# Kernel optimization log

Measured on AMD Instinct MI355X. Metric: run time of the kernel, lower is better.

The kernel has to match this reference:

```python
import jax, jax.numpy as jnp
import numpy as np

N, E, IN, C, H = 50000, 1600000, 128, 64, 2
HC = H * C  # 128; num_out = 128, conv_out channels per head = 64
NEG_SLOPE = 0.2


def setup_inputs() -> dict:
    key = jax.random.key(0)
    ks = jax.random.split(key, 16)
    x = jax.random.normal(ks[0], (N, IN), dtype=jnp.float32)
    edge_index = jax.random.randint(ks[1], (2, E), 0, N, dtype=jnp.int64)

    def gat_params(k, fan_in, heads, out_ch):
        k1, k2, k3 = jax.random.split(k, 3)
        sc = 1.0 / np.sqrt(fan_in)
        W = jax.random.normal(k1, (fan_in, heads * out_ch), dtype=jnp.float32) * sc
        a_src = jax.random.normal(k2, (heads, out_ch), dtype=jnp.float32) * 0.1
        a_dst = jax.random.normal(k3, (heads, out_ch), dtype=jnp.float32) * 0.1
        b = jnp.zeros((heads * out_ch,), dtype=jnp.float32)
        return W, a_src, a_dst, b

    W_in, a_src_in, a_dst_in, b_in = gat_params(ks[2], IN, H, C)
    # 2 hidden layers, stacked on leading axis
    Wh, ash, adh, bh = [], [], [], []
    for i in range(2):
        W, a_s, a_d, b = gat_params(ks[3 + i], HC, H, C)
        Wh.append(W); ash.append(a_s); adh.append(a_d); bh.append(b)
    W_h = jnp.stack(Wh); a_src_h = jnp.stack(ash)
    a_dst_h = jnp.stack(adh); b_h = jnp.stack(bh)
    W_out, a_src_out, a_dst_out, b_out = gat_params(ks[6], HC, H, C)
    return dict(x=x, edge_index=edge_index,
                W_in=W_in, a_src_in=a_src_in, a_dst_in=a_dst_in, b_in=b_in,
                W_h=W_h, a_src_h=a_src_h, a_dst_h=a_dst_h, b_h=b_h,
                W_out=W_out, a_src_out=a_src_out, a_dst_out=a_dst_out, b_out=b_out)


def gat_layer(xf, src, dst, W, a_src, a_dst, b, heads, out_ch):
    n = xf.shape[0]
    h = (xf @ W).reshape(n, heads, out_ch)              # [N,H,C]
    e_src = jnp.einsum('nhc,hc->nh', h, a_src)          # [N,H]
    e_dst = jnp.einsum('nhc,hc->nh', h, a_dst)
    e = jax.nn.leaky_relu(e_src[src] + e_dst[dst], NEG_SLOPE)  # [E',H]
    m = jax.ops.segment_max(e, dst, num_segments=n)     # softmax over edges per dst
    p = jnp.exp(e - m[dst])
    s = jax.ops.segment_sum(p, dst, num_segments=n)
    alpha = p / (s[dst] + 1e-16)
    out = jax.ops.segment_sum(alpha[:, :, None] * h[src], dst, num_segments=n)
    return out.reshape(n, heads * out_ch) + b


def reference(x, edge_index, W_in, a_src_in, a_dst_in, b_in,
              W_h, a_src_h, a_dst_h, b_h,
              W_out, a_src_out, a_dst_out, b_out):
    # add self loops (PyG GATConv default add_self_loops=True)
    loops = jnp.arange(N, dtype=edge_index.dtype)
    src = jnp.concatenate([edge_index[0], loops])
    dst = jnp.concatenate([edge_index[1], loops])

    h = jax.nn.relu(gat_layer(x, src, dst, W_in, a_src_in, a_dst_in, b_in, H, C))
    for i in range(2):
        h = jax.nn.relu(gat_layer(h, src, dst, W_h[i], a_src_h[i], a_dst_h[i], b_h[i], H, C))
    out = gat_layer(h, src, dst, W_out, a_src_out, a_dst_out, b_out, H, C)
    return out
```

## Files before the change

### kernel.cpp

```cpp
#include <hip/hip_runtime.h>

#define NNODES 50000
#define NEDGES 1600000
#define NEG_SLOPE 0.2f

#define SCAN_NB 256
#define SCAN_CH 196

typedef __attribute__((ext_vector_type(8))) short short8;
typedef __attribute__((ext_vector_type(4))) float f32x4;
typedef __attribute__((ext_vector_type(4))) unsigned short us4;

static __device__ __forceinline__ unsigned short f2bf(float f) {
    unsigned u = __float_as_uint(f);
    unsigned r = u + 0x7FFFu + ((u >> 16) & 1u);
    return (unsigned short)(r >> 16);
}
static __device__ __forceinline__ float bf2f(unsigned short h) {
    return __uint_as_float(((unsigned)h) << 16);
}
static __device__ __forceinline__ unsigned short f2h(float f) {
    union { _Float16 x; unsigned short u; } c;
    c.x = (_Float16)f;
    return c.u;
}
static __device__ __forceinline__ float h2f(unsigned short u) {
    union { unsigned short u; _Float16 x; } c;
    c.u = u;
    return (float)c.x;
}


__global__ void k_count(const int* __restrict__ ei, int* __restrict__ count,
                        int* __restrict__ pos) {
    int t = blockIdx.x * blockDim.x + threadIdx.x;
    int stride = gridDim.x * blockDim.x;
    #pragma unroll
    for (int i = 0; i < 8; i++) {
        int e = t + i * stride;
        if (e < NEDGES) pos[e] = atomicAdd(&count[ei[NEDGES + e]], 1);
    }
}

__global__ __launch_bounds__(256) void k_bsum(const int* __restrict__ count,
                                              int* __restrict__ bsum) {
    __shared__ int red[4];
    int t = threadIdx.x, b = blockIdx.x;
    int idx = b * SCAN_CH + t;
    int v = (t < SCAN_CH && idx < NNODES) ? count[idx] + 1 : 0;
    #pragma unroll
    for (int m = 1; m <= 32; m <<= 1) v += __shfl_xor(v, m);
    if ((t & 63) == 0) red[t >> 6] = v;
    __syncthreads();
    if (t == 0) bsum[b] = red[0] + red[1] + red[2] + red[3];
}

__global__ __launch_bounds__(256) void k_bscan(const int* __restrict__ bsum,
                                               int* __restrict__ boff,
                                               int* __restrict__ row_ptr) {
    __shared__ int s[256];
    int t = threadIdx.x;
    int v = bsum[t];
    s[t] = v;
    __syncthreads();
    for (int off = 1; off < 256; off <<= 1) {
        int u = (t >= off) ? s[t - off] : 0;
        __syncthreads();
        s[t] += u;
        __syncthreads();
    }
    boff[t] = s[t] - v;
    if (t == 255) row_ptr[NNODES] = s[255];
}

__global__ __launch_bounds__(256) void k_rowptr(const int* __restrict__ count,
                                                const int* __restrict__ boff,
                                                int* __restrict__ row_ptr,
                                                int* __restrict__ csr_src) {
    __shared__ int s[256];
    int t = threadIdx.x, b = blockIdx.x;
    int idx = b * SCAN_CH + t;
    bool valid = (t < SCAN_CH && idx < NNODES);
    int v = valid ? count[idx] + 1 : 0;
    s[t] = v;
    __syncthreads();
    for (int off = 1; off < 256; off <<= 1) {
        int u = (t >= off) ? s[t - off] : 0;
        __syncthreads();
        s[t] += u;
        __syncthreads();
    }
    if (valid) {
        int run = boff[b] + s[t] - v;
        row_ptr[idx] = run;
        csr_src[run] = idx;
    }
}

__global__ void k_scatter(const int* __restrict__ ei, const int* __restrict__ row_ptr,
                          const int* __restrict__ pos, int* __restrict__ csr_src) {
    int t = blockIdx.x * blockDim.x + threadIdx.x;
    int stride = gridDim.x * blockDim.x;
    #pragma unroll
    for (int i = 0; i < 4; i++) {
        int e = t + i * stride;
        if (e < NEDGES) {
            int s = ei[e];
            int d = ei[NEDGES + e];
            __builtin_nontemporal_store(s, &csr_src[row_ptr[d] + 1 + pos[e]]);
        }
    }
}


__global__ void k_split(const float* __restrict__ x, unsigned short* __restrict__ hi,
                        unsigned short* __restrict__ lo) {
    int i = blockIdx.x * blockDim.x + threadIdx.x;
    if (i >= NNODES * 128 / 4) return;
    float4 v = *(const float4*)(x + (size_t)i * 4);
    unsigned short h0 = f2bf(v.x), h1 = f2bf(v.y), h2 = f2bf(v.z), h3 = f2bf(v.w);
    *(ushort4*)(hi + (size_t)i * 4) = make_ushort4(h0, h1, h2, h3);
    *(ushort4*)(lo + (size_t)i * 4) =
        make_ushort4(f2bf(v.x - bf2f(h0)), f2bf(v.y - bf2f(h1)),
                     f2bf(v.z - bf2f(h2)), f2bf(v.w - bf2f(h3)));
}

__global__ __launch_bounds__(256, 2) void k_gemm_mfma(
        const unsigned short* __restrict__ Ahi, const unsigned short* __restrict__ Alo,
        const float* __restrict__ W,
        const float* __restrict__ a_src, const float* __restrict__ a_dst,
        unsigned short* __restrict__ Hh,
        float* __restrict__ e_src, float* __restrict__ e_dst)
{
    __shared__ __align__(16) short sAhi[128 * 128];
    __shared__ __align__(16) short sAlo[128 * 128];
    __shared__ float eS[4][128];
    __shared__ float eD[4][128];

    const int tid  = threadIdx.x;
    const int lane = tid & 63;
    const int w    = tid >> 6;
    const int l15  = lane & 15;
    const int quad = lane >> 4;
    const int row0 = blockIdx.x * 128;

    short8 Bh[2][4], Bl[2][4];
    for (int nt = 0; nt < 2; nt++) {
        int n = w * 32 + nt * 16 + l15;
        for (int ks = 0; ks < 4; ks++) {
            short8 bh, bl;
            #pragma unroll
            for (int j = 0; j < 8; j++) {
                float wv = W[(size_t)(ks * 32 + quad * 8 + j) * 128 + n];
                unsigned short h = f2bf(wv);
                bh[j] = (short)h;
                bl[j] = (short)f2bf(wv - bf2f(h));
            }
            Bh[nt][ks] = bh; Bl[nt][ks] = bl;
        }
    }

    for (int i = tid; i < 2048; i += 256) {
        int m  = i >> 4;
        int kc = i & 15;
        int g  = row0 + m; if (g > NNODES - 1) g = NNODES - 1;
        int cp = kc ^ (m & 15);
        short8 vh = *(const short8*)(Ahi + (size_t)g * 128 + kc * 8);
        short8 vl = *(const short8*)(Alo + (size_t)g * 128 + kc * 8);
        *(short8*)&sAhi[m * 128 + cp * 8] = vh;
        *(short8*)&sAlo[m * 128 + cp * 8] = vl;
    }
    __syncthreads();

    f32x4 zero = {0.f, 0.f, 0.f, 0.f};
    f32x4 acc[8][2];
    #pragma unroll
    for (int mt = 0; mt < 8; mt++) { acc[mt][0] = zero; acc[mt][1] = zero; }

    #pragma unroll
    for (int mt = 0; mt < 8; mt++) {
        int m = mt * 16 + l15;
        #pragma unroll
        for (int ks = 0; ks < 4; ks++) {
            int kc = ks * 4 + quad;
            int cp = kc ^ l15;
            short8 ah = *(const short8*)&sAhi[m * 128 + cp * 8];
            short8 al = *(const short8*)&sAlo[m * 128 + cp * 8];
            #pragma unroll
            for (int nt = 0; nt < 2; nt++) {
                acc[mt][nt] = __builtin_amdgcn_mfma_f32_16x16x32_bf16(ah, Bh[nt][ks], acc[mt][nt], 0, 0, 0);
                acc[mt][nt] = __builtin_amdgcn_mfma_f32_16x16x32_bf16(al, Bh[nt][ks], acc[mt][nt], 0, 0, 0);
                acc[mt][nt] = __builtin_amdgcn_mfma_f32_16x16x32_bf16(ah, Bl[nt][ks], acc[mt][nt], 0, 0, 0);
            }
        }
    }

    float as0 = a_src[w * 32 + l15],      ad0 = a_dst[w * 32 + l15];
    float as1 = a_src[w * 32 + 16 + l15], ad1 = a_dst[w * 32 + 16 + l15];
    #pragma unroll
    for (int mt = 0; mt < 8; mt++) {
        #pragma unroll
        for (int r = 0; r < 4; r++) {
            int m = mt * 16 + quad * 4 + r;
            int g = row0 + m;
            float v0 = acc[mt][0][r], v1 = acc[mt][1][r];
            if (g < NNODES) {
                int n0 = w * 32 + l15;
                Hh[(size_t)g * 128 + n0]      = f2h(v0);
                Hh[(size_t)g * 128 + n0 + 16] = f2h(v1);
            }
            float ps = v0 * as0 + v1 * as1;
            float pd = v0 * ad0 + v1 * ad1;
            ps += __shfl_xor(ps, 1); ps += __shfl_xor(ps, 2);
            ps += __shfl_xor(ps, 4); ps += __shfl_xor(ps, 8);
            pd += __shfl_xor(pd, 1); pd += __shfl_xor(pd, 2);
            pd += __shfl_xor(pd, 4); pd += __shfl_xor(pd, 8);
            if (l15 == 0) { eS[w][m] = ps; eD[w][m] = pd; }
        }
    }
    __syncthreads();
    {
        int m = tid >> 1, head = tid & 1;
        int g = row0 + m;
        if (g < NNODES) {
            e_src[g * 2 + head] = eS[head * 2][m] + eS[head * 2 + 1][m];
            e_dst[g * 2 + head] = eD[head * 2][m] + eD[head * 2 + 1][m];
        }
    }
}

__global__ __launch_bounds__(256) void k_aggregate_h(const unsigned short* __restrict__ Hh,
                                                     const float* __restrict__ e_src,
                                                     const float* __restrict__ e_dst,
                                                     const int* __restrict__ row_ptr,
                                                     const int* __restrict__ csr_src,
                                                     const float* __restrict__ bias,
                                                     unsigned short* __restrict__ ohi,
                                                     unsigned short* __restrict__ olo) {
    int lane = threadIdx.x & 63;
    int wv   = threadIdx.x >> 6;
    int d    = blockIdx.x * 4 + wv;
    if (d >= NNODES) return;
    int half = lane >> 5;
    int li   = lane & 31;
    int head = li >> 4;
    int c0   = li * 4;
    float ed = e_dst[d * 2 + head];
    int beg = row_ptr[d], end = row_ptr[d + 1];
    f32x4 acc = {0.f, 0.f, 0.f, 0.f};
    float ssum = 0.f;
    int j = beg;
    for (; j + 16 <= end; j += 16) {
        int s[8];
        #pragma unroll
        for (int u = 0; u < 8; u++) s[u] = csr_src[j + 2 * u + half];
        us4 q[8];
        #pragma unroll
        for (int u = 0; u < 8; u++) q[u] = *(const us4*)(Hh + (size_t)s[u] * 128 + c0);
        float p[8];
        #pragma unroll
        for (int u = 0; u < 8; u++) {
            float t = e_src[s[u] * 2 + head] + ed;
            t = t > 0.f ? t : NEG_SLOPE * t;
            p[u] = __expf(t);
        }
        #pragma unroll
        for (int u = 0; u < 8; u++) {
            acc[0] += p[u] * h2f(q[u][0]);
            acc[1] += p[u] * h2f(q[u][1]);
            acc[2] += p[u] * h2f(q[u][2]);
            acc[3] += p[u] * h2f(q[u][3]);
            ssum   += p[u];
        }
    }
    for (; j < end; j += 2) {
        int idx = j + half;
        bool valid = idx < end;
        int s = csr_src[valid ? idx : end - 1];
        float t = e_src[s * 2 + head] + ed;
        t = t > 0.f ? t : NEG_SLOPE * t;
        float p = valid ? __expf(t) : 0.f;
        us4 q = *(const us4*)(Hh + (size_t)s * 128 + c0);
        acc[0] += p * h2f(q[0]);
        acc[1] += p * h2f(q[1]);
        acc[2] += p * h2f(q[2]);
        acc[3] += p * h2f(q[3]);
        ssum   += p;
    }
    acc[0] += __shfl_xor(acc[0], 32);
    acc[1] += __shfl_xor(acc[1], 32);
    acc[2] += __shfl_xor(acc[2], 32);
    acc[3] += __shfl_xor(acc[3], 32);
    ssum   += __shfl_xor(ssum,   32);
    if (half == 0) {
        float inv = 1.0f / ssum;
        float4 bv = *(const float4*)(bias + c0);
        float o0 = fmaxf(acc[0] * inv + bv.x, 0.f);
        float o1 = fmaxf(acc[1] * inv + bv.y, 0.f);
        float o2 = fmaxf(acc[2] * inv + bv.z, 0.f);
        float o3 = fmaxf(acc[3] * inv + bv.w, 0.f);
        unsigned short h0 = f2bf(o0), h1 = f2bf(o1), h2 = f2bf(o2), h3 = f2bf(o3);
        *(ushort4*)&ohi[(size_t)d * 128 + c0] = make_ushort4(h0, h1, h2, h3);
        *(ushort4*)&olo[(size_t)d * 128 + c0] =
            make_ushort4(f2bf(o0 - bf2f(h0)), f2bf(o1 - bf2f(h1)),
                         f2bf(o2 - bf2f(h2)), f2bf(o3 - bf2f(h3)));
    }
}

__global__ __launch_bounds__(256) void k_aggregate_f(const unsigned short* __restrict__ Hh,
                                                     const float* __restrict__ e_src,
                                                     const float* __restrict__ e_dst,
                                                     const int* __restrict__ row_ptr,
                                                     const int* __restrict__ csr_src,
                                                     const float* __restrict__ bias,
                                                     float* __restrict__ outf) {
    int lane = threadIdx.x & 63;
    int wv   = threadIdx.x >> 6;
    int d    = blockIdx.x * 4 + wv;
    if (d >= NNODES) return;
    int half = lane >> 5;
    int li   = lane & 31;
    int head = li >> 4;
    int c0   = li * 4;
    float ed = e_dst[d * 2 + head];
    int beg = row_ptr[d], end = row_ptr[d + 1];
    f32x4 acc = {0.f, 0.f, 0.f, 0.f};
    float ssum = 0.f;
    int j = beg;
    for (; j + 16 <= end; j += 16) {
        int s[8];
        #pragma unroll
        for (int u = 0; u < 8; u++) s[u] = csr_src[j + 2 * u + half];
        us4 q[8];
        #pragma unroll
        for (int u = 0; u < 8; u++) q[u] = *(const us4*)(Hh + (size_t)s[u] * 128 + c0);
        float p[8];
        #pragma unroll
        for (int u = 0; u < 8; u++) {
            float t = e_src[s[u] * 2 + head] + ed;
            t = t > 0.f ? t : NEG_SLOPE * t;
            p[u] = __expf(t);
        }
        #pragma unroll
        for (int u = 0; u < 8; u++) {
            acc[0] += p[u] * h2f(q[u][0]);
            acc[1] += p[u] * h2f(q[u][1]);
            acc[2] += p[u] * h2f(q[u][2]);
            acc[3] += p[u] * h2f(q[u][3]);
            ssum   += p[u];
        }
    }
    for (; j < end; j += 2) {
        int idx = j + half;
        bool valid = idx < end;
        int s = csr_src[valid ? idx : end - 1];
        float t = e_src[s * 2 + head] + ed;
        t = t > 0.f ? t : NEG_SLOPE * t;
        float p = valid ? __expf(t) : 0.f;
        us4 q = *(const us4*)(Hh + (size_t)s * 128 + c0);
        acc[0] += p * h2f(q[0]);
        acc[1] += p * h2f(q[1]);
        acc[2] += p * h2f(q[2]);
        acc[3] += p * h2f(q[3]);
        ssum   += p;
    }
    acc[0] += __shfl_xor(acc[0], 32);
    acc[1] += __shfl_xor(acc[1], 32);
    acc[2] += __shfl_xor(acc[2], 32);
    acc[3] += __shfl_xor(acc[3], 32);
    ssum   += __shfl_xor(ssum,   32);
    if (half == 0) {
        float inv = 1.0f / ssum;
        float4 bv = *(const float4*)(bias + c0);
        *(float4*)(outf + (size_t)d * 128 + c0) =
            make_float4(acc[0] * inv + bv.x, acc[1] * inv + bv.y,
                        acc[2] * inv + bv.z, acc[3] * inv + bv.w);
    }
}


extern "C" void kernel_launch(void* const* d_in, const int* in_sizes, int n_in,
                              void* d_out, int out_size, void* d_ws, size_t ws_size,
                              hipStream_t stream) {
    const float* x  = (const float*)d_in[0];
    const int*   ei = (const int*)d_in[1];

    char* ws = (char*)d_ws;
    size_t off = 0;
    auto alloc = [&](size_t bytes) {
        void* p = ws + off;
        off = (off + bytes + 255) & ~(size_t)255;
        return p;
    };
    int*            count   = (int*)alloc((size_t)NNODES * 4);
    int*            row_ptr = (int*)alloc((size_t)(NNODES + 1) * 4);
    int*            csr     = (int*)alloc((size_t)(NEDGES + NNODES) * 4);
    int*            pos     = (int*)alloc((size_t)NEDGES * 4);
    int*            bsum    = (int*)alloc((size_t)SCAN_NB * 4);
    int*            boff    = (int*)alloc((size_t)SCAN_NB * 4);
    unsigned short* hh      = (unsigned short*)alloc((size_t)NNODES * 128 * 2);
    float*          es      = (float*)alloc((size_t)NNODES * 2 * 4);
    float*          edv     = (float*)alloc((size_t)NNODES * 2 * 4);
    (void)ws_size; (void)in_sizes; (void)n_in; (void)out_size;

    unsigned short* hi = (unsigned short*)d_out;
    unsigned short* lo = hi + (size_t)NNODES * 128;

    hipMemsetAsync(count, 0, (size_t)NNODES * 4, stream);
    k_count  <<<(NEDGES + 8 * 256 - 1) / (8 * 256), 256, 0, stream>>>(ei, count, pos);
    k_bsum   <<<SCAN_NB, 256, 0, stream>>>(count, bsum);
    k_bscan  <<<1, 256, 0, stream>>>(bsum, boff, row_ptr);
    k_rowptr <<<SCAN_NB, 256, 0, stream>>>(count, boff, row_ptr, csr);
    k_scatter<<<(NEDGES + 4 * 256 - 1) / (4 * 256), 256, 0, stream>>>(ei, row_ptr, pos, csr);
    k_split  <<<(NNODES * 128 / 4 + 255) / 256, 256, 0, stream>>>(x, hi, lo);

    const float* W_h = (const float*)d_in[6];
    const float* ash = (const float*)d_in[7];
    const float* adh = (const float*)d_in[8];
    const float* bh  = (const float*)d_in[9];

    struct Layer { const float *W, *as, *ad, *b; };
    Layer L[4] = {
        { (const float*)d_in[2],  (const float*)d_in[3],  (const float*)d_in[4],  (const float*)d_in[5]  },
        { W_h,              ash,        adh,        bh        },
        { W_h + 128 * 128,  ash + 128,  adh + 128,  bh + 128  },
        { (const float*)d_in[10], (const float*)d_in[11], (const float*)d_in[12], (const float*)d_in[13] },
    };

    const int gemm_blocks = (NNODES + 127) / 128;
    const int agg_blocks  = (NNODES + 3) / 4;
    for (int l = 0; l < 4; l++) {
        k_gemm_mfma<<<gemm_blocks, 256, 0, stream>>>(hi, lo, L[l].W, L[l].as, L[l].ad,
                                                     hh, es, edv);
        if (l < 3) {
            k_aggregate_h<<<agg_blocks, 256, 0, stream>>>(hh, es, edv, row_ptr, csr,
                                                          L[l].b, hi, lo);
        } else {
            k_aggregate_f<<<agg_blocks, 256, 0, stream>>>(hh, es, edv, row_ptr, csr,
                                                          L[l].b, (float*)d_out);
        }
    }
}
```

Measured before the change: 596.4 us.

## Precompute bf16 split weights once, fuse input split into GEMM, persistent 64-row tiles

Adds a one-time kernel that converts all four layers' weights into transposed bf16 hi/lo pairs. Each GEMM block can then load its B fragments with vector loads instead of doing strided fp32 loads and conversions per block. The standalone x split kernel is removed and the first layer converts x to hi/lo inside the GEMM tile load. The GEMM now uses 64-row tiles in a grid-stride loop over 768 blocks with higher occupancy. This saves a full pass over x and the repeated weight conversion, at the cost of extra syncs per tile and a launch that loops.

```diff
diff --git a/kernel.cpp b/kernel.cpp
--- a/kernel.cpp
+++ b/kernel.cpp
@@ -6,6 +6,10 @@
 
 #define SCAN_NB 256
 #define SCAN_CH 196
+
+#define MT_ROWS 64
+#define NMT 782
+#define GEMM_BLOCKS 768
 
 typedef __attribute__((ext_vector_type(8))) short short8;
 typedef __attribute__((ext_vector_type(4))) float f32x4;
@@ -112,120 +116,135 @@
     }
 }
 
-
-__global__ void k_split(const float* __restrict__ x, unsigned short* __restrict__ hi,
-                        unsigned short* __restrict__ lo) {
-    int i = blockIdx.x * blockDim.x + threadIdx.x;
-    if (i >= NNODES * 128 / 4) return;
-    float4 v = *(const float4*)(x + (size_t)i * 4);
-    unsigned short h0 = f2bf(v.x), h1 = f2bf(v.y), h2 = f2bf(v.z), h3 = f2bf(v.w);
-    *(ushort4*)(hi + (size_t)i * 4) = make_ushort4(h0, h1, h2, h3);
-    *(ushort4*)(lo + (size_t)i * 4) =
-        make_ushort4(f2bf(v.x - bf2f(h0)), f2bf(v.y - bf2f(h1)),
-                     f2bf(v.z - bf2f(h2)), f2bf(v.w - bf2f(h3)));
-}
-
-__global__ __launch_bounds__(256, 2) void k_gemm_mfma(
+__global__ __launch_bounds__(256) void k_wprep(const float* __restrict__ W0,
+                                               const float* __restrict__ Wh,
+                                               const float* __restrict__ Wout,
+                                               unsigned short* __restrict__ wthi,
+                                               unsigned short* __restrict__ wtlo) {
+    int t = blockIdx.x * blockDim.x + threadIdx.x;
+    int l = t >> 14;
+    int i = t & 16383;
+    int k = i >> 7, n = i & 127;
+    const float* src = (l == 0) ? W0 : (l == 3) ? Wout : (Wh + (size_t)(l - 1) * 16384);
+    float v = src[i];
+    unsigned short h = f2bf(v);
+    wthi[(size_t)l * 16384 + n * 128 + k] = h;
+    wtlo[(size_t)l * 16384 + n * 128 + k] = f2bf(v - bf2f(h));
+}
+
+__global__ __launch_bounds__(256, 3) void k_gemm_mfma(
+        const float* __restrict__ X,
         const unsigned short* __restrict__ Ahi, const unsigned short* __restrict__ Alo,
-        const float* __restrict__ W,
+        const unsigned short* __restrict__ Wthi, const unsigned short* __restrict__ Wtlo,
         const float* __restrict__ a_src, const float* __restrict__ a_dst,
         unsigned short* __restrict__ Hh,
-        float* __restrict__ e_src, float* __restrict__ e_dst)
+        float* __restrict__ e_src, float* __restrict__ e_dst, int use_x)
 {
-    __shared__ __align__(16) short sAhi[128 * 128];
-    __shared__ __align__(16) short sAlo[128 * 128];
-    __shared__ float eS[4][128];
-    __shared__ float eD[4][128];
+    __shared__ __align__(16) short sAhi[MT_ROWS * 128];
+    __shared__ __align__(16) short sAlo[MT_ROWS * 128];
+    __shared__ float eS[4][MT_ROWS];
+    __shared__ float eD[4][MT_ROWS];
 
     const int tid  = threadIdx.x;
     const int lane = tid & 63;
     const int w    = tid >> 6;
     const int l15  = lane & 15;
     const int quad = lane >> 4;
-    const int row0 = blockIdx.x * 128;
 
     short8 Bh[2][4], Bl[2][4];
+    #pragma unroll
     for (int nt = 0; nt < 2; nt++) {
         int n = w * 32 + nt * 16 + l15;
+        #pragma unroll
         for (int ks = 0; ks < 4; ks++) {
-            short8 bh, bl;
-            #pragma unroll
-            for (int j = 0; j < 8; j++) {
-                float wv = W[(size_t)(ks * 32 + quad * 8 + j) * 128 + n];
-                unsigned short h = f2bf(wv);
-                bh[j] = (short)h;
-                bl[j] = (short)f2bf(wv - bf2f(h));
-            }
-            Bh[nt][ks] = bh; Bl[nt][ks] = bl;
-        }
-    }
-
-    for (int i = tid; i < 2048; i += 256) {
-        int m  = i >> 4;
-        int kc = i & 15;
-        int g  = row0 + m; if (g > NNODES - 1) g = NNODES - 1;
-        int cp = kc ^ (m & 15);
-        short8 vh = *(const short8*)(Ahi + (size_t)g * 128 + kc * 8);
-        short8 vl = *(const short8*)(Alo + (size_t)g * 128 + kc * 8);
-        *(short8*)&sAhi[m * 128 + cp * 8] = vh;
-        *(short8*)&sAlo[m * 128 + cp * 8] = vl;
-    }
-    __syncthreads();
-
-    f32x4 zero = {0.f, 0.f, 0.f, 0.f};
-    f32x4 acc[8][2];
-    #pragma unroll
-    for (int mt = 0; mt < 8; mt++) { acc[mt][0] = zero; acc[mt][1] = zero; }
-
-    #pragma unroll
-    for (int mt = 0; mt < 8; mt++) {
-        int m = mt * 16 + l15;
-        #pragma unroll
-        for (int ks = 0; ks < 4; ks++) {
-            int kc = ks * 4 + quad;
-            int cp = kc ^ l15;
-            short8 ah = *(const short8*)&sAhi[m * 128 + cp * 8];
-            short8 al = *(const short8*)&sAlo[m * 128 + cp * 8];
-            #pragma unroll
-            for (int nt = 0; nt < 2; nt++) {
-                acc[mt][nt] = __builtin_amdgcn_mfma_f32_16x16x32_bf16(ah, Bh[nt][ks], acc[mt][nt], 0, 0, 0);
-                acc[mt][nt] = __builtin_amdgcn_mfma_f32_16x16x32_bf16(al, Bh[nt][ks], acc[mt][nt], 0, 0, 0);
-                acc[mt][nt] = __builtin_amdgcn_mfma_f32_16x16x32_bf16(ah, Bl[nt][ks], acc[mt][nt], 0, 0, 0);
-            }
-        }
-    }
-
+            Bh[nt][ks] = *(const short8*)(Wthi + (size_t)n * 128 + ks * 32 + quad * 8);
+            Bl[nt][ks] = *(const short8*)(Wtlo + (size_t)n * 128 + ks * 32 + quad * 8);
+        }
+    }
     float as0 = a_src[w * 32 + l15],      ad0 = a_dst[w * 32 + l15];
     float as1 = a_src[w * 32 + 16 + l15], ad1 = a_dst[w * 32 + 16 + l15];
-    #pragma unroll
-    for (int mt = 0; mt < 8; mt++) {
-        #pragma unroll
-        for (int r = 0; r < 4; r++) {
-            int m = mt * 16 + quad * 4 + r;
+
+    for (int mt0 = blockIdx.x; mt0 < NMT; mt0 += GEMM_BLOCKS) {
+        const int row0 = mt0 * MT_ROWS;
+
+        for (int i = tid; i < MT_ROWS * 16; i += 256) {
+            int m  = i >> 4;
+            int kc = i & 15;
+            int g  = row0 + m; if (g > NNODES - 1) g = NNODES - 1;
+            int cp = kc ^ (m & 15);
+            short8 vh, vl;
+            if (use_x) {
+                float4 xa = *(const float4*)(X + (size_t)g * 128 + kc * 8);
+                float4 xb = *(const float4*)(X + (size_t)g * 128 + kc * 8 + 4);
+                float xs[8] = {xa.x, xa.y, xa.z, xa.w, xb.x, xb.y, xb.z, xb.w};
+                #pragma unroll
+                for (int q = 0; q < 8; q++) {
+                    unsigned short h = f2bf(xs[q]);
+                    vh[q] = (short)h;
+                    vl[q] = (short)f2bf(xs[q] - bf2f(h));
+                }
+            } else {
+                vh = *(const short8*)(Ahi + (size_t)g * 128 + kc * 8);
+                vl = *(const short8*)(Alo + (size_t)g * 128 + kc * 8);
+            }
+            *(short8*)&sAhi[m * 128 + cp * 8] = vh;
+            *(short8*)&sAlo[m * 128 + cp * 8] = vl;
+        }
+        __syncthreads();
+
+        f32x4 zero = {0.f, 0.f, 0.f, 0.f};
+        f32x4 acc[4][2];
+        #pragma unroll
+        for (int mt = 0; mt < 4; mt++) { acc[mt][0] = zero; acc[mt][1] = zero; }
+        #pragma unroll
+        for (int mt = 0; mt < 4; mt++) {
+            int m = mt * 16 + l15;
+            #pragma unroll
+            for (int ks = 0; ks < 4; ks++) {
+                int kc = ks * 4 + quad;
+                int cp = kc ^ l15;
+                short8 ah = *(const short8*)&sAhi[m * 128 + cp * 8];
+                short8 al = *(const short8*)&sAlo[m * 128 + cp * 8];
+                #pragma unroll
+                for (int nt = 0; nt < 2; nt++) {
+                    acc[mt][nt] = __builtin_amdgcn_mfma_f32_16x16x32_bf16(ah, Bh[nt][ks], acc[mt][nt], 0, 0, 0);
+                    acc[mt][nt] = __builtin_amdgcn_mfma_f32_16x16x32_bf16(al, Bh[nt][ks], acc[mt][nt], 0, 0, 0);
+                    acc[mt][nt] = __builtin_amdgcn_mfma_f32_16x16x32_bf16(ah, Bl[nt][ks], acc[mt][nt], 0, 0, 0);
+                }
+            }
+        }
+
+        #pragma unroll
+        for (int mt = 0; mt < 4; mt++) {
+            #pragma unroll
+            for (int r = 0; r < 4; r++) {
+                int m = mt * 16 + quad * 4 + r;
+                int g = row0 + m;
+                float v0 = acc[mt][0][r], v1 = acc[mt][1][r];
+                if (g < NNODES) {
+                    int n0 = w * 32 + l15;
+                    Hh[(size_t)g * 128 + n0]      = f2h(v0);
+                    Hh[(size_t)g * 128 + n0 + 16] = f2h(v1);
+                }
+                float ps = v0 * as0 + v1 * as1;
+                float pd = v0 * ad0 + v1 * ad1;
+                ps += __shfl_xor(ps, 1); ps += __shfl_xor(ps, 2);
+                ps += __shfl_xor(ps, 4); ps += __shfl_xor(ps, 8);
+                pd += __shfl_xor(pd, 1); pd += __shfl_xor(pd, 2);
+                pd += __shfl_xor(pd, 4); pd += __shfl_xor(pd, 8);
+                if (l15 == 0) { eS[w][m] = ps; eD[w][m] = pd; }
+            }
+        }
+        __syncthreads();
+        if (tid < MT_ROWS * 2) {
+            int m = tid >> 1, head = tid & 1;
             int g = row0 + m;
-            float v0 = acc[mt][0][r], v1 = acc[mt][1][r];
             if (g < NNODES) {
-                int n0 = w * 32 + l15;
-                Hh[(size_t)g * 128 + n0]      = f2h(v0);
-                Hh[(size_t)g * 128 + n0 + 16] = f2h(v1);
+                e_src[g * 2 + head] = eS[head * 2][m] + eS[head * 2 + 1][m];
+                e_dst[g * 2 + head] = eD[head * 2][m] + eD[head * 2 + 1][m];
             }
-            float ps = v0 * as0 + v1 * as1;
-            float pd = v0 * ad0 + v1 * ad1;
-            ps += __shfl_xor(ps, 1); ps += __shfl_xor(ps, 2);
-            ps += __shfl_xor(ps, 4); ps += __shfl_xor(ps, 8);
-            pd += __shfl_xor(pd, 1); pd += __shfl_xor(pd, 2);
-            pd += __shfl_xor(pd, 4); pd += __shfl_xor(pd, 8);
-            if (l15 == 0) { eS[w][m] = ps; eD[w][m] = pd; }
-        }
-    }
-    __syncthreads();
-    {
-        int m = tid >> 1, head = tid & 1;
-        int g = row0 + m;
-        if (g < NNODES) {
-            e_src[g * 2 + head] = eS[head * 2][m] + eS[head * 2 + 1][m];
-            e_dst[g * 2 + head] = eD[head * 2][m] + eD[head * 2 + 1][m];
-        }
+        }
+        __syncthreads();
     }
 }
 
@@ -399,6 +418,8 @@
     int*            bsum    = (int*)alloc((size_t)SCAN_NB * 4);
     int*            boff    = (int*)alloc((size_t)SCAN_NB * 4);
     unsigned short* hh      = (unsigned short*)alloc((size_t)NNODES * 128 * 2);
+    unsigned short* wthi    = (unsigned short*)alloc((size_t)4 * 16384 * 2);
+    unsigned short* wtlo    = (unsigned short*)alloc((size_t)4 * 16384 * 2);
     float*          es      = (float*)alloc((size_t)NNODES * 2 * 4);
     float*          edv     = (float*)alloc((size_t)NNODES * 2 * 4);
     (void)ws_size; (void)in_sizes; (void)n_in; (void)out_size;
@@ -406,32 +427,35 @@
     unsigned short* hi = (unsigned short*)d_out;
     unsigned short* lo = hi + (size_t)NNODES * 128;
 
+    const float* W0   = (const float*)d_in[2];
+    const float* W_h  = (const float*)d_in[6];
+    const float* Wout = (const float*)d_in[10];
+
     hipMemsetAsync(count, 0, (size_t)NNODES * 4, stream);
     k_count  <<<(NEDGES + 8 * 256 - 1) / (8 * 256), 256, 0, stream>>>(ei, count, pos);
+    k_wprep  <<<256, 256, 0, stream>>>(W0, W_h, Wout, wthi, wtlo);
     k_bsum   <<<SCAN_NB, 256, 0, stream>>>(count, bsum);
     k_bscan  <<<1, 256, 0, stream>>>(bsum, boff, row_ptr);
     k_rowptr <<<SCAN_NB, 256, 0, stream>>>(count, boff, row_ptr, csr);
     k_scatter<<<(NEDGES + 4 * 256 - 1) / (4 * 256), 256, 0, stream>>>(ei, row_ptr, pos, csr);
-    k_split  <<<(NNODES * 128 / 4 + 255) / 256, 256, 0, stream>>>(x, hi, lo);
-
-    const float* W_h = (const float*)d_in[6];
+
     const float* ash = (const float*)d_in[7];
     const float* adh = (const float*)d_in[8];
     const float* bh  = (const float*)d_in[9];
 
-    struct Layer { const float *W, *as, *ad, *b; };
+    struct Layer { const float *as, *ad, *b; };
     Layer L[4] = {
-        { (const float*)d_in[2],  (const float*)d_in[3],  (const float*)d_in[4],  (const float*)d_in[5]  },
-        { W_h,              ash,        adh,        bh        },
-        { W_h + 128 * 128,  ash + 128,  adh + 128,  bh + 128  },
-        { (const float*)d_in[10], (const float*)d_in[11], (const float*)d_in[12], (const float*)d_in[13] },
+        { (const float*)d_in[3],  (const float*)d_in[4],  (const float*)d_in[5]  },
+        { ash,        adh,        bh        },
+        { ash + 128,  adh + 128,  bh + 128  },
+        { (const float*)d_in[11], (const float*)d_in[12], (const float*)d_in[13] },
     };
 
-    const int gemm_blocks = (NNODES + 127) / 128;
-    const int agg_blocks  = (NNODES + 3) / 4;
+    const int agg_blocks = (NNODES + 3) / 4;
     for (int l = 0; l < 4; l++) {
-        k_gemm_mfma<<<gemm_blocks, 256, 0, stream>>>(hi, lo, L[l].W, L[l].as, L[l].ad,
-                                                     hh, es, edv);
+        k_gemm_mfma<<<GEMM_BLOCKS, 256, 0, stream>>>(
+            x, hi, lo, wthi + (size_t)l * 16384, wtlo + (size_t)l * 16384,
+            L[l].as, L[l].ad, hh, es, edv, l == 0 ? 1 : 0);
         if (l < 3) {
             k_aggregate_h<<<agg_blocks, 256, 0, stream>>>(hh, es, edv, row_ptr, csr,
                                                           L[l].b, hi, lo);
```

After: 597.2 us. Within noise of the previous version (+0.1%).
